# Optimization experiments

Hardware: AMD Instinct MI355X
Metric: run time of the kernel (lower is better)

Reference implementation:

```python
import jax, jax.numpy as jnp
import numpy as np

H = 16      # num_head
D = 1024    # feat_dim
DK = D // H # per-head dim
B, S = 2, 2048


def setup_inputs() -> dict:
    key = jax.random.key(0)
    ks = jax.random.split(key, 11)
    scale = 1.0 / np.sqrt(D)
    inp = {
        'query': jax.random.normal(ks[0], (B, S, D), jnp.float32),
        'key':   jax.random.normal(ks[1], (B, S, D), jnp.float32),
        'value': jax.random.normal(ks[2], (B, S, D), jnp.float32),
        # causal lower-triangular mask (seq, seq); 0 entries get -1e9
        'mask':  jnp.tril(jnp.ones((S, S), jnp.int32)),
        # torch nn.Linear params: y = x @ W.T + b
        'w_q': jax.random.normal(ks[3], (D, D), jnp.float32) * scale,
        'b_q': jax.random.normal(ks[4], (D,), jnp.float32) * scale,
        'w_k': jax.random.normal(ks[5], (D, D), jnp.float32) * scale,
        'b_k': jax.random.normal(ks[6], (D,), jnp.float32) * scale,
        'w_v': jax.random.normal(ks[7], (D, D), jnp.float32) * scale,
        'b_v': jax.random.normal(ks[8], (D,), jnp.float32) * scale,
        'w_out': jax.random.normal(ks[9], (D, D), jnp.float32) * scale,
        'b_out': jax.random.normal(ks[10], (D,), jnp.float32) * scale,
    }
    return inp


def reference(query, key, value, mask, w_q, b_q, w_k, b_k, w_v, b_v, w_out, b_out):
    b = query.shape[0]
    # projections + split heads -> (b, h, s, d_k)
    def proj(x, w, bias):
        y = x @ w.T + bias
        return y.reshape(b, -1, H, DK).transpose(0, 2, 1, 3)
    q = proj(query, w_q, b_q)
    k = proj(key, w_k, b_k)
    v = proj(value, w_v, b_v)
    # scaled dot-product attention with materialized score matrix
    scores = jnp.einsum('bhqd,bhkd->bhqk', q, k) / np.sqrt(DK).astype(jnp.float32)
    scores = jnp.where(mask == 0, jnp.float32(-1e9), scores)
    attn = jax.nn.softmax(scores, axis=-1)  # dropout is identity in eval mode
    x = jnp.einsum('bhqk,bhkd->bhqd', attn, v)
    x = x.transpose(0, 2, 1, 3).reshape(b, -1, H * DK)
    return x @ w_out.T + b_out
```

## Files before the change

kernel.cpp:

```cpp
#include <hip/hip_runtime.h>

typedef unsigned short u16;
typedef __attribute__((ext_vector_type(8))) short short8;
typedef __attribute__((ext_vector_type(8))) unsigned short u16x8;
typedef __attribute__((ext_vector_type(4))) float floatx4;

#define S2LOG 0.18033688f

__device__ __forceinline__ u16 f2bf(float f) {
    unsigned int u = __float_as_uint(f);
    return (u16)((u + 0x7FFFu + ((u >> 16) & 1u)) >> 16);
}
__device__ __forceinline__ u16 f2bf_hu(float f) {
    return (u16)((__float_as_uint(f) + 0x8000u) >> 16);
}
__device__ __forceinline__ void gl_lds16(const u16* g, u16* l) {
    __builtin_amdgcn_global_load_lds(
        (const __attribute__((address_space(1))) void*)g,
        (__attribute__((address_space(3))) void*)l, 16, 0, 0);
}

__global__ __launch_bounds__(256) void cvt_all(
    const float* __restrict__ q, const float* __restrict__ k, const float* __restrict__ v,
    const float* __restrict__ wq, const float* __restrict__ wk,
    const float* __restrict__ wv, const float* __restrict__ wo,
    u16* __restrict__ ws)
{
    const int b = blockIdx.x, t = threadIdx.x;
    const float* src; u16* dst; long blk;
    if      (b < 2048) { src = q;  dst = ws;            blk = b; }
    else if (b < 4096) { src = k;  dst = ws + 4194304;  blk = b - 2048; }
    else if (b < 6144) { src = v;  dst = ws + 8388608;  blk = b - 4096; }
    else if (b < 6656) { src = wq; dst = ws + 12582912; blk = b - 6144; }
    else if (b < 7168) { src = wk; dst = ws + 13631488; blk = b - 6656; }
    else if (b < 7680) { src = wv; dst = ws + 14680064; blk = b - 7168; }
    else               { src = wo; dst = ws + 15728640; blk = b - 7680; }
    const long i = blk * 2048 + (long)t * 8;
    const float4 a = *(const float4*)(src + i);
    const float4 c = *(const float4*)(src + i + 4);
    u16x8 o;
    o[0] = f2bf(a.x); o[1] = f2bf(a.y); o[2] = f2bf(a.z); o[3] = f2bf(a.w);
    o[4] = f2bf(c.x); o[5] = f2bf(c.y); o[6] = f2bf(c.z); o[7] = f2bf(c.w);
    *(u16x8*)(dst + i) = o;
}

__device__ __forceinline__ void gemm_core64(
    const u16* __restrict__ A, const u16* __restrict__ Bw,
    int m0, int n0, floatx4 (&acc)[2][4])
{
    __shared__ u16 As[128 * 64];
    __shared__ u16 Bs[64 * 64];
    const int t = threadIdx.x, w = t >> 6;
    const int lane = t & 63, col = lane & 15, quad = lane >> 4;
    const int c7 = col & 7;

#pragma unroll
    for (int i = 0; i < 2; ++i)
#pragma unroll
        for (int j = 0; j < 4; ++j) acc[i][j] = (floatx4)0.f;

    for (int k0 = 0; k0 < 1024; k0 += 64) {
#pragma unroll
        for (int jj = 0; jj < 4; ++jj) {
            const int c = jj * 256 + t;
            const int row = c >> 3, kc = (c & 7) ^ (row & 7);
            gl_lds16(A + (size_t)(m0 + row) * 1024 + k0 + kc * 8,
                     As + (jj * 256 + w * 64) * 8);
        }
#pragma unroll
        for (int jj = 0; jj < 2; ++jj) {
            const int c = jj * 256 + t;
            const int row = c >> 3, kc = (c & 7) ^ (row & 7);
            gl_lds16(Bw + (size_t)(n0 + row) * 1024 + k0 + kc * 8,
                     Bs + (jj * 256 + w * 64) * 8);
        }
        __syncthreads();
#pragma unroll
        for (int ks = 0; ks < 2; ++ks) {
            const int swz = (ks * 4 + quad) ^ c7;
            short8 af[2], bf[4];
#pragma unroll
            for (int i = 0; i < 2; ++i)
                af[i] = *(const short8*)&As[((w * 32 + i * 16 + col) * 8 + swz) * 8];
#pragma unroll
            for (int j = 0; j < 4; ++j)
                bf[j] = *(const short8*)&Bs[((j * 16 + col) * 8 + swz) * 8];
#pragma unroll
            for (int i = 0; i < 2; ++i)
#pragma unroll
                for (int j = 0; j < 4; ++j)
                    acc[i][j] = __builtin_amdgcn_mfma_f32_16x16x32_bf16(
                        af[i], bf[j], acc[i][j], 0, 0, 0);
        }
        __syncthreads();
    }
}

__global__ __launch_bounds__(256) void gemm_qkv(
    const u16* __restrict__ xq, const u16* __restrict__ xk, const u16* __restrict__ xv,
    const u16* __restrict__ wqb, const u16* __restrict__ wkb, const u16* __restrict__ wvb,
    const float* __restrict__ bq, const float* __restrict__ bk, const float* __restrict__ bv,
    u16* __restrict__ Qh, u16* __restrict__ Kh, u16* __restrict__ Vt)
{
    const int z = blockIdx.z;
    const u16*   A    = z == 0 ? xq  : z == 1 ? xk  : xv;
    const u16*   Bw   = z == 0 ? wqb : z == 1 ? wkb : wvb;
    const float* bias = z == 0 ? bq  : z == 1 ? bk  : bv;
    u16*         out  = z == 0 ? Qh  : z == 1 ? Kh  : Vt;
    const float  scale = z == 0 ? S2LOG : 1.0f;
    const int m0 = blockIdx.x * 128, n0 = blockIdx.y * 64;

    floatx4 acc[2][4];
    gemm_core64(A, Bw, m0, n0, acc);

    const int t = threadIdx.x, w = t >> 6;
    const int lane = t & 63, col = lane & 15, quad = lane >> 4;
#pragma unroll
    for (int i = 0; i < 2; ++i)
#pragma unroll
        for (int j = 0; j < 4; ++j)
#pragma unroll
            for (int reg = 0; reg < 4; ++reg) {
                const int gm = m0 + w * 32 + i * 16 + quad * 4 + reg;
                const int gn = n0 + j * 16 + col;
                const float val = (acc[i][j][reg] + bias[gn]) * scale;
                const int bb = gm >> 11, ss = gm & 2047, hh = gn >> 6, dd = gn & 63;
                if (z != 2)
                    out[(((size_t)bb * 16 + hh) * 2048 + ss) * 64 + dd] = f2bf(val);
                else
                    out[(((size_t)bb * 16 + hh) * 64 + dd) * 2048 + ss] = f2bf(val);
            }
}

__global__ __launch_bounds__(256) void gemm_out(
    const u16* __restrict__ A, const u16* __restrict__ Bw,
    const float* __restrict__ bias, float* __restrict__ out)
{
    const int m0 = blockIdx.x * 128, n0 = blockIdx.y * 64;
    floatx4 acc[2][4];
    gemm_core64(A, Bw, m0, n0, acc);
    const int t = threadIdx.x, w = t >> 6;
    const int lane = t & 63, col = lane & 15, quad = lane >> 4;
#pragma unroll
    for (int i = 0; i < 2; ++i)
#pragma unroll
        for (int j = 0; j < 4; ++j)
#pragma unroll
            for (int reg = 0; reg < 4; ++reg) {
                const int gm = m0 + w * 32 + i * 16 + quad * 4 + reg;
                const int gn = n0 + j * 16 + col;
                out[(size_t)gm * 1024 + gn] = acc[i][j][reg] + bias[gn];
            }
}

__global__ __launch_bounds__(256) void attn_mfma(
    const u16* __restrict__ Qh, const u16* __restrict__ Kh,
    const u16* __restrict__ Vt, u16* __restrict__ ctx)
{
    __shared__ u16 QPs[128 * 64];
    __shared__ u16 Ks[3][64 * 64];
    __shared__ u16 Vs[3][64 * 64];
    const int t = threadIdx.x, w = t >> 6;
    const int lane = t & 63, col = lane & 15, quad = lane >> 4;
    const int c7 = col & 7;
    const int bh = blockIdx.y;
    const int qt = (bh < 16) ? (15 - (int)blockIdx.x) : (int)blockIdx.x;
    const int q0 = qt * 128;
    const u16* qg = Qh + ((size_t)bh * 2048 + q0) * 64;
    const u16* kg = Kh + (size_t)bh * 2048 * 64;
    const u16* vg = Vt + (size_t)bh * 2048 * 64;

    auto stage = [&](int tile, int buf) {
#pragma unroll
        for (int jj = 0; jj < 2; ++jj) {
            const int c = jj * 256 + t;
            const int row = c >> 3, kc = (c & 7) ^ (row & 7);
            gl_lds16(kg + (size_t)(tile * 64 + row) * 64 + kc * 8,
                     Ks[buf] + (jj * 256 + w * 64) * 8);
            gl_lds16(vg + (size_t)row * 2048 + tile * 64 + kc * 8,
                     Vs[buf] + (jj * 256 + w * 64) * 8);
        }
    };

#pragma unroll
    for (int jj = 0; jj < 4; ++jj) {
        const int c = jj * 256 + t;
        const int row = c >> 3, kc = (c & 7) ^ (row & 7);
        gl_lds16(qg + (size_t)row * 64 + kc * 8, QPs + (jj * 256 + w * 64) * 8);
    }
    stage(0, 0);
    stage(1, 1);
    asm volatile("s_waitcnt vmcnt(4)" ::: "memory");
    __builtin_amdgcn_s_barrier();

    short8 qf[2][2];
#pragma unroll
    for (int i = 0; i < 2; ++i)
#pragma unroll
        for (int ks = 0; ks < 2; ++ks)
            qf[i][ks] = *(const short8*)
                &QPs[((w * 32 + i * 16 + col) * 8 + ((ks * 4 + quad) ^ c7)) * 8];
    asm volatile("s_waitcnt lgkmcnt(0)" ::: "memory");
    __builtin_amdgcn_s_barrier();

    floatx4 oacc[2][4], lacc[2];
#pragma unroll
    for (int i = 0; i < 2; ++i) {
        lacc[i] = (floatx4)0.f;
#pragma unroll
        for (int j = 0; j < 4; ++j) oacc[i][j] = (floatx4)0.f;
    }
    short8 ones;
#pragma unroll
    for (int i = 0; i < 8; ++i) ones[i] = (short)0x3F80;

    const int ktmax = 2 * qt + 1;
    int cur = 0, stb = 2;
    for (int kt = 0; kt <= ktmax; ++kt) {
        if (kt + 2 <= ktmax) stage(kt + 2, stb);

        floatx4 sa[2][4];
#pragma unroll
        for (int i = 0; i < 2; ++i)
#pragma unroll
            for (int j = 0; j < 4; ++j) sa[i][j] = (floatx4)0.f;
#pragma unroll
        for (int ks = 0; ks < 2; ++ks) {
            const int swz = (ks * 4 + quad) ^ c7;
            short8 kf[4];
#pragma unroll
            for (int jc = 0; jc < 4; ++jc)
                kf[jc] = *(const short8*)&Ks[cur][((jc * 16 + col) * 8 + swz) * 8];
#pragma unroll
            for (int i = 0; i < 2; ++i)
#pragma unroll
                for (int jc = 0; jc < 4; ++jc)
                    sa[i][jc] = __builtin_amdgcn_mfma_f32_16x16x32_bf16(
                        qf[i][ks], kf[jc], sa[i][jc], 0, 0, 0);
        }
        const bool pm = (kt >= 2 * qt);
#pragma unroll
        for (int i = 0; i < 2; ++i)
#pragma unroll
            for (int reg = 0; reg < 4; ++reg) {
                const int prow = w * 32 + i * 16 + quad * 4 + reg;
                const int qrow = q0 + prow;
                const int pr7 = (quad * 4 + reg) & 7;
                u16* pr = &QPs[prow * 64 + (col & 7)];
#pragma unroll
                for (int jc = 0; jc < 4; ++jc) {
                    float p = __builtin_amdgcn_exp2f(sa[i][jc][reg]);
                    if (pm && (kt * 64 + jc * 16 + col > qrow)) p = 0.f;
                    pr[((2 * jc + (col >> 3)) ^ pr7) << 3] = f2bf_hu(p);
                }
            }
#pragma unroll
        for (int ks = 0; ks < 2; ++ks) {
            const int swz = (ks * 4 + quad) ^ c7;
            short8 pf[2], vf[4];
#pragma unroll
            for (int i = 0; i < 2; ++i)
                pf[i] = *(const short8*)
                    &QPs[((w * 32 + i * 16 + col) * 8 + swz) * 8];
#pragma unroll
            for (int jd = 0; jd < 4; ++jd)
                vf[jd] = *(const short8*)&Vs[cur][((jd * 16 + col) * 8 + swz) * 8];
#pragma unroll
            for (int i = 0; i < 2; ++i) {
                lacc[i] = __builtin_amdgcn_mfma_f32_16x16x32_bf16(pf[i], ones, lacc[i], 0, 0, 0);
#pragma unroll
                for (int jd = 0; jd < 4; ++jd)
                    oacc[i][jd] = __builtin_amdgcn_mfma_f32_16x16x32_bf16(
                        pf[i], vf[jd], oacc[i][jd], 0, 0, 0);
            }
        }
        asm volatile("s_waitcnt vmcnt(4) lgkmcnt(0)" ::: "memory");
        __builtin_amdgcn_s_barrier();
        cur = (cur == 2) ? 0 : cur + 1;
        stb = (stb == 2) ? 0 : stb + 1;
    }

    const int bb = bh >> 4, hh = bh & 15;
#pragma unroll
    for (int i = 0; i < 2; ++i)
#pragma unroll
        for (int reg = 0; reg < 4; ++reg) {
            const float inv = __builtin_amdgcn_rcpf(lacc[i][reg]);
            const int qrow = q0 + w * 32 + i * 16 + quad * 4 + reg;
#pragma unroll
            for (int jd = 0; jd < 4; ++jd)
                ctx[((size_t)bb * 2048 + qrow) * 1024 + hh * 64 + jd * 16 + col] =
                    f2bf(oacc[i][jd][reg] * inv);
        }
}

extern "C" void kernel_launch(void* const* d_in, const int* in_sizes, int n_in,
                              void* d_out, int out_size, void* d_ws, size_t ws_size,
                              hipStream_t stream)
{
    const float* query = (const float*)d_in[0];
    const float* key   = (const float*)d_in[1];
    const float* value = (const float*)d_in[2];
    const float* w_q   = (const float*)d_in[4];
    const float* b_q   = (const float*)d_in[5];
    const float* w_k   = (const float*)d_in[6];
    const float* b_k   = (const float*)d_in[7];
    const float* w_v   = (const float*)d_in[8];
    const float* b_v   = (const float*)d_in[9];
    const float* w_out = (const float*)d_in[10];
    const float* b_out = (const float*)d_in[11];

    u16* W = (u16*)d_ws;
    u16* xq  = W;
    u16* xk  = W + 4194304;
    u16* xv  = W + 8388608;
    u16* wqb = W + 12582912;
    u16* wkb = W + 13631488;
    u16* wvb = W + 14680064;
    u16* wob = W + 15728640;
    u16* Qh  = W + 16777216;
    u16* Kh  = W + 20971520;
    u16* Vtw = W + 25165824;
    u16* ctx = W + 29360128;

    hipLaunchKernelGGL(cvt_all, dim3(8192), dim3(256), 0, stream,
                       query, key, value, w_q, w_k, w_v, w_out, W);

    hipLaunchKernelGGL(gemm_qkv, dim3(32, 16, 3), dim3(256), 0, stream,
                       xq, xk, xv, wqb, wkb, wvb, b_q, b_k, b_v, Qh, Kh, Vtw);

    hipLaunchKernelGGL(attn_mfma, dim3(16, 32), dim3(256), 0, stream, Qh, Kh, Vtw, ctx);

    hipLaunchKernelGGL(gemm_out, dim3(32, 16), dim3(256), 0, stream,
                       ctx, wob, b_out, (float*)d_out);
}
```

Baseline: 234.7 us.

## Use 128x128 tiles for QKV GEMM and double-buffer attention K/V

Adds a 128x128 GEMM core in which each wave computes a 64x64 sub-tile, and uses it for the QKV projection with half as many N blocks. This raises operand reuse per LDS load and cuts global traffic, at the cost of more accumulator registers and fewer blocks. Separately, the attention kernel drops from triple to double buffering of K/V tiles with a full vmcnt(0) wait and barrier at the top of each iteration. That lowers LDS use and may allow more resident blocks, but exposes more load latency because prefetch runs only one tile ahead.

```diff
diff --git a/kernel.cpp b/kernel.cpp
--- a/kernel.cpp
+++ b/kernel.cpp
@@ -96,6 +96,54 @@
     }
 }
 
+__device__ __forceinline__ void gemm_core128(
+    const u16* __restrict__ A, const u16* __restrict__ Bw,
+    int m0, int n0, floatx4 (&acc)[4][4])
+{
+    __shared__ u16 As[128 * 64];
+    __shared__ u16 Bs[128 * 64];
+    const int t = threadIdx.x, w = t >> 6;
+    const int lane = t & 63, col = lane & 15, quad = lane >> 4;
+    const int c7 = col & 7;
+    const int wr = (w >> 1) * 64, wc = (w & 1) * 64;
+
+#pragma unroll
+    for (int i = 0; i < 4; ++i)
+#pragma unroll
+        for (int j = 0; j < 4; ++j) acc[i][j] = (floatx4)0.f;
+
+    for (int k0 = 0; k0 < 1024; k0 += 64) {
+#pragma unroll
+        for (int jj = 0; jj < 4; ++jj) {
+            const int c = jj * 256 + t;
+            const int row = c >> 3, kc = (c & 7) ^ (row & 7);
+            gl_lds16(A + (size_t)(m0 + row) * 1024 + k0 + kc * 8,
+                     As + (jj * 256 + w * 64) * 8);
+            gl_lds16(Bw + (size_t)(n0 + row) * 1024 + k0 + kc * 8,
+                     Bs + (jj * 256 + w * 64) * 8);
+        }
+        __syncthreads();
+#pragma unroll
+        for (int ks = 0; ks < 2; ++ks) {
+            const int swz = (ks * 4 + quad) ^ c7;
+            short8 af[4], bf[4];
+#pragma unroll
+            for (int i = 0; i < 4; ++i)
+                af[i] = *(const short8*)&As[((wr + i * 16 + col) * 8 + swz) * 8];
+#pragma unroll
+            for (int j = 0; j < 4; ++j)
+                bf[j] = *(const short8*)&Bs[((wc + j * 16 + col) * 8 + swz) * 8];
+#pragma unroll
+            for (int i = 0; i < 4; ++i)
+#pragma unroll
+                for (int j = 0; j < 4; ++j)
+                    acc[i][j] = __builtin_amdgcn_mfma_f32_16x16x32_bf16(
+                        af[i], bf[j], acc[i][j], 0, 0, 0);
+        }
+        __syncthreads();
+    }
+}
+
 __global__ __launch_bounds__(256) void gemm_qkv(
     const u16* __restrict__ xq, const u16* __restrict__ xk, const u16* __restrict__ xv,
     const u16* __restrict__ wqb, const u16* __restrict__ wkb, const u16* __restrict__ wvb,
@@ -108,21 +156,22 @@
     const float* bias = z == 0 ? bq  : z == 1 ? bk  : bv;
     u16*         out  = z == 0 ? Qh  : z == 1 ? Kh  : Vt;
     const float  scale = z == 0 ? S2LOG : 1.0f;
-    const int m0 = blockIdx.x * 128, n0 = blockIdx.y * 64;
-
-    floatx4 acc[2][4];
-    gemm_core64(A, Bw, m0, n0, acc);
-
-    const int t = threadIdx.x, w = t >> 6;
-    const int lane = t & 63, col = lane & 15, quad = lane >> 4;
-#pragma unroll
-    for (int i = 0; i < 2; ++i)
+    const int m0 = blockIdx.x * 128, n0 = blockIdx.y * 128;
+
+    floatx4 acc[4][4];
+    gemm_core128(A, Bw, m0, n0, acc);
+
+    const int t = threadIdx.x, w = t >> 6;
+    const int lane = t & 63, col = lane & 15, quad = lane >> 4;
+    const int wr = (w >> 1) * 64, wc = (w & 1) * 64;
+#pragma unroll
+    for (int i = 0; i < 4; ++i)
 #pragma unroll
         for (int j = 0; j < 4; ++j)
 #pragma unroll
             for (int reg = 0; reg < 4; ++reg) {
-                const int gm = m0 + w * 32 + i * 16 + quad * 4 + reg;
-                const int gn = n0 + j * 16 + col;
+                const int gm = m0 + wr + i * 16 + quad * 4 + reg;
+                const int gn = n0 + wc + j * 16 + col;
                 const float val = (acc[i][j][reg] + bias[gn]) * scale;
                 const int bb = gm >> 11, ss = gm & 2047, hh = gn >> 6, dd = gn & 63;
                 if (z != 2)
@@ -158,8 +207,8 @@
     const u16* __restrict__ Vt, u16* __restrict__ ctx)
 {
     __shared__ u16 QPs[128 * 64];
-    __shared__ u16 Ks[3][64 * 64];
-    __shared__ u16 Vs[3][64 * 64];
+    __shared__ u16 Ks[2][64 * 64];
+    __shared__ u16 Vs[2][64 * 64];
     const int t = threadIdx.x, w = t >> 6;
     const int lane = t & 63, col = lane & 15, quad = lane >> 4;
     const int c7 = col & 7;
@@ -189,7 +238,6 @@
         gl_lds16(qg + (size_t)row * 64 + kc * 8, QPs + (jj * 256 + w * 64) * 8);
     }
     stage(0, 0);
-    stage(1, 1);
     asm volatile("s_waitcnt vmcnt(4)" ::: "memory");
     __builtin_amdgcn_s_barrier();
 
@@ -215,9 +263,11 @@
     for (int i = 0; i < 8; ++i) ones[i] = (short)0x3F80;
 
     const int ktmax = 2 * qt + 1;
-    int cur = 0, stb = 2;
+    int cur = 0;
     for (int kt = 0; kt <= ktmax; ++kt) {
-        if (kt + 2 <= ktmax) stage(kt + 2, stb);
+        asm volatile("s_waitcnt vmcnt(0)" ::: "memory");
+        __builtin_amdgcn_s_barrier();
+        if (kt + 1 <= ktmax) stage(kt + 1, cur ^ 1);
 
         floatx4 sa[2][4];
 #pragma unroll
@@ -274,10 +324,7 @@
                         pf[i], vf[jd], oacc[i][jd], 0, 0, 0);
             }
         }
-        asm volatile("s_waitcnt vmcnt(4) lgkmcnt(0)" ::: "memory");
-        __builtin_amdgcn_s_barrier();
-        cur = (cur == 2) ? 0 : cur + 1;
-        stb = (stb == 2) ? 0 : stb + 1;
+        cur ^= 1;
     }
 
     const int bb = bh >> 4, hh = bh & 15;
@@ -326,7 +373,7 @@
     hipLaunchKernelGGL(cvt_all, dim3(8192), dim3(256), 0, stream,
                        query, key, value, w_q, w_k, w_v, w_out, W);
 
-    hipLaunchKernelGGL(gemm_qkv, dim3(32, 16, 3), dim3(256), 0, stream,
+    hipLaunchKernelGGL(gemm_qkv, dim3(32, 8, 3), dim3(256), 0, stream,
                        xq, xk, xv, wqb, wkb, wvb, b_q, b_k, b_v, Qh, Kh, Vtw);
 
     hipLaunchKernelGGL(attn_mfma, dim3(16, 32), dim3(256), 0, stream, Qh, Kh, Vtw, ctx);
```

Measured after the change: 248.2 us. 5.8% more time.
